# Optimization experiments

Measured on AMD Instinct MI355X. Metric: run time of the kernel, lower is better.

## Reference

```python
import jax, jax.numpy as jnp
import numpy as np

B, S, NB = 8, 512, 23
INIT, E, R, T = 512, 256, 3, 2
NEG = -9e8

def _gru(x, h, wih, whh, bih, bhh):
    gi = x @ wih.T + bih
    gh = h @ whh.T + bhh
    ir, iz, inn = jnp.split(gi, 3, axis=-1)
    hr, hz, hn = jnp.split(gh, 3, axis=-1)
    r = jax.nn.sigmoid(ir + hr)
    z = jax.nn.sigmoid(iz + hz)
    n = jnp.tanh(inn + r * hn)
    return (1.0 - z) * n + z * h

def setup_inputs():
    key = jax.random.key(0)
    ks = jax.random.split(key, 30)
    def lin(k, o, i):
        return jax.random.normal(k, (o, i), jnp.float32) * 0.02
    def vec(k, n):
        return jax.random.normal(k, (n,), jnp.float32) * 0.02
    inp = {}
    inp["amino_list"] = jax.random.normal(ks[0], (B, S, INIT), jnp.float32)
    inp["amino_mask"] = (jax.random.uniform(ks[1], (B, S)) < 0.9).astype(jnp.float32)
    inp["emb_W"] = lin(ks[2], E, INIT); inp["emb_b"] = vec(ks[3], E)
    inp["nb_W"] = lin(ks[4], E, INIT); inp["nb_b"] = vec(ks[5], E)
    inp["align_W"] = jax.random.normal(ks[6], (R, 1, 2 * E), jnp.float32) * 0.02
    inp["align_b"] = jax.random.normal(ks[7], (R, 1), jnp.float32) * 0.02
    inp["attend_W"] = jax.random.normal(ks[8], (R, E, E), jnp.float32) * 0.02
    inp["attend_b"] = jax.random.normal(ks[9], (R, E), jnp.float32) * 0.02
    inp["gru_wih"] = jax.random.normal(ks[10], (R, 3 * E, E), jnp.float32) * 0.02
    inp["gru_whh"] = jax.random.normal(ks[11], (R, 3 * E, E), jnp.float32) * 0.02
    inp["gru_bih"] = jax.random.normal(ks[12], (R, 3 * E), jnp.float32) * 0.02
    inp["gru_bhh"] = jax.random.normal(ks[13], (R, 3 * E), jnp.float32) * 0.02
    inp["seq_align_W"] = lin(ks[14], 1, 2 * E); inp["seq_align_b"] = vec(ks[15], 1)
    inp["seq_attend_W"] = lin(ks[16], E, E); inp["seq_attend_b"] = vec(ks[17], E)
    inp["seq_gru_wih"] = lin(ks[18], 3 * E, E); inp["seq_gru_bih"] = vec(ks[19], 3 * E)
    inp["seq_gru_whh"] = lin(ks[20], 3 * E, E); inp["seq_gru_bhh"] = vec(ks[21], 3 * E)
    inp["amino_degree_list"] = jax.random.randint(ks[22], (B, S, NB), -1, S)
    return inp

def reference(amino_list, amino_mask, emb_W, emb_b, nb_W, nb_b, align_W, align_b,
              attend_W, attend_b, gru_wih, gru_whh, gru_bih, gru_bhh,
              seq_align_W, seq_align_b, seq_attend_W, seq_attend_b,
              seq_gru_wih, seq_gru_whh, seq_gru_bih, seq_gru_bhh, amino_degree_list):
    idx = amino_degree_list
    lrelu = jax.nn.leaky_relu
    # per-batch neighbor gather: (S,D),(S,NB) -> (S,NB,D); index -1 wraps (masked out below)
    gather = jax.vmap(lambda f, i: f[i])
    feat = lrelu(amino_list @ emb_W.T + emb_b)               # (B,S,E)
    nfeat = lrelu(gather(amino_list, idx) @ nb_W.T + nb_b)   # (B,S,NB,E)
    attend_mask = (idx != -1).astype(feat.dtype)             # (B,S,NB)
    smask = jnp.where(idx == -1, NEG, 0.0).astype(feat.dtype)

    def attn(d, center, nbr):
        # align Linear on concat([center, nbr]) split into two matvecs (same math, no concat)
        aW = align_W[d, 0]
        score = lrelu(jnp.einsum('bse,e->bs', center, aW[:E])[:, :, None]
                      + jnp.einsum('bsne,e->bsn', nbr, aW[E:]) + align_b[d, 0])
        w = jax.nn.softmax(score + smask, axis=-1) * attend_mask   # softmax over neighbor axis
        nt = nbr @ attend_W[d].T + attend_b[d]
        return jax.nn.elu(jnp.einsum('bsn,bsne->bse', w, nt))

    h = _gru(attn(0, feat, nfeat).reshape(-1, E), feat.reshape(-1, E),
             gru_wih[0], gru_whh[0], gru_bih[0], gru_bhh[0])
    act = jax.nn.relu(h.reshape(B, S, E))
    for d in range(1, R):
        ctx = attn(d, act, gather(act, idx))
        h = _gru(ctx.reshape(-1, E), h, gru_wih[d], gru_whh[d], gru_bih[d], gru_bhh[d])
        act = jax.nn.relu(h.reshape(B, S, E))

    seq_feature = jnp.sum(act * amino_mask[:, :, None], axis=1)  # (B,E)
    act_mol = jax.nn.relu(seq_feature)                           # fixed across T (as in torch)
    seq_smask = jnp.where(amino_mask == 0, NEG, 0.0)
    saW = seq_align_W[0]
    act_seq = act_mol
    for _ in range(T):
        score = lrelu((act_mol @ saW[:E])[:, None]
                      + jnp.einsum('bse,e->bs', act, saW[E:]) + seq_align_b[0])
        w = jax.nn.softmax(score + seq_smask, axis=-1) * amino_mask  # softmax over seq axis
        tf = act @ seq_attend_W.T + seq_attend_b
        seq_ctx = jax.nn.elu(jnp.einsum('bs,bse->be', w, tf))
        seq_feature = _gru(seq_ctx, seq_feature, seq_gru_wih, seq_gru_whh, seq_gru_bih, seq_gru_bhh)
        act_seq = jax.nn.relu(seq_feature)
    return (act_seq, act)
```

## Files before the change

kernel.cpp:

```cpp
#include <hip/hip_runtime.h>
#include <math.h>


#define BSZ   8
#define SEQ   512
#define NBR   23
#define EMB   256
#define INITD 512
#define BS    (BSZ*SEQ)
#define G3    (3*EMB)
#define NEGV  -9e8f

typedef __attribute__((ext_vector_type(8))) short short8;
typedef __attribute__((ext_vector_type(4))) float f32x4;

__device__ __forceinline__ float lrelu(float x){ return x > 0.f ? x : 0.01f*x; }
__device__ __forceinline__ float elu1 (float x){ return x > 0.f ? x : (expf(x)-1.f); }
__device__ __forceinline__ float sigm (float x){ return 1.f/(1.f+expf(-x)); }
__device__ __forceinline__ float bf2f(ushort u){
    union { unsigned int i; float f; } v; v.i = ((unsigned int)u) << 16; return v.f;
}
__device__ __forceinline__ ushort f2bf(float f){
    union { float f; unsigned int i; } v; v.f = f;
    unsigned int u = v.i;
    return (ushort)((u + 0x7FFFu + ((u >> 16) & 1u)) >> 16);
}
__device__ __forceinline__ unsigned pk2(float a, float b){
    return (unsigned)f2bf(a) | ((unsigned)f2bf(b) << 16);
}
__device__ __forceinline__ void unpack8(uint4 v, float* o) {
    o[0]=bf2f((ushort)(v.x&0xffff)); o[1]=bf2f((ushort)(v.x>>16));
    o[2]=bf2f((ushort)(v.y&0xffff)); o[3]=bf2f((ushort)(v.y>>16));
    o[4]=bf2f((ushort)(v.z&0xffff)); o[5]=bf2f((ushort)(v.z>>16));
    o[6]=bf2f((ushort)(v.w&0xffff)); o[7]=bf2f((ushort)(v.w>>16));
}

__device__ __forceinline__ void gload_lds16(const void* g, void* l) {
    __builtin_amdgcn_global_load_lds(
        (const __attribute__((address_space(1))) unsigned int*)g,
        (__attribute__((address_space(3))) unsigned int*)l,
        16, 0, 0);
}

__global__ __launch_bounds__(256) void convert_flat(
    const float* __restrict__ amino, ushort* __restrict__ aminobf,
    const float* __restrict__ embW,  ushort* __restrict__ embWbf,
    const float* __restrict__ nbW,   ushort* __restrict__ nbWbf,
    const float* __restrict__ attW,  ushort* __restrict__ attWbf,
    const float* __restrict__ gwih,  ushort* __restrict__ gwihbf,
    const float* __restrict__ gwhh,  ushort* __restrict__ gwhhbf,
    const float* __restrict__ satW,  ushort* __restrict__ satWbf,
    const float* __restrict__ sgwih, ushort* __restrict__ sgwihbf,
    const float* __restrict__ sgwhh, ushort* __restrict__ sgwhhbf,
    float* __restrict__ seqfeatZ)
{
    const unsigned stride = gridDim.x * 256;
    for (unsigned u = blockIdx.x*256 + threadIdx.x; u < 524544u; u += stride) {
        const float* s; ushort* d; unsigned lu;
        if      (u < 262144u) { s=amino; d=aminobf; lu=u; }
        else if (u < 278528u) { s=embW;  d=embWbf;  lu=u-262144u; }
        else if (u < 294912u) { s=nbW;   d=nbWbf;   lu=u-278528u; }
        else if (u < 319488u) { s=attW;  d=attWbf;  lu=u-294912u; }
        else if (u < 393216u) { s=gwih;  d=gwihbf;  lu=u-319488u; }
        else if (u < 466944u) { s=gwhh;  d=gwhhbf;  lu=u-393216u; }
        else if (u < 475136u) { s=satW;  d=satWbf;  lu=u-466944u; }
        else if (u < 499712u) { s=sgwih; d=sgwihbf; lu=u-475136u; }
        else if (u < 524288u) { s=sgwhh; d=sgwhhbf; lu=u-499712u; }
        else {
            unsigned i = (u - 524288u) * 8;
            *reinterpret_cast<float4*>(&seqfeatZ[i])     = make_float4(0,0,0,0);
            *reinterpret_cast<float4*>(&seqfeatZ[i + 4]) = make_float4(0,0,0,0);
            continue;
        }
        size_t i = (size_t)lu * 8;
        float4 a = *reinterpret_cast<const float4*>(s + i);
        float4 b = *reinterpret_cast<const float4*>(s + i + 4);
        uint4 o;
        o.x = pk2(a.x, a.y); o.y = pk2(a.z, a.w);
        o.z = pk2(b.x, b.y); o.w = pk2(b.z, b.w);
        *reinterpret_cast<uint4*>(d + i) = o;
    }
}

struct GemmLds64 { ushort A[2][128][64]; ushort B[2][64][64]; };

template<int ACT>
__device__ __forceinline__ void gemm64_dev(
    const ushort* __restrict__ A, const ushort* __restrict__ W,
    const float* __restrict__ bias,
    float* __restrict__ C, ushort* __restrict__ Cbf,
    int N, int K, int bx, int by, GemmLds64& L)
{
    const int tid = threadIdx.x;
    const int m0 = bx * 128, n0 = by * 64;
    const int wv = tid >> 6, lane = tid & 63;
    const int fr = lane & 15, grp = lane >> 4;
    const int kc = K >> 3;
    const int mh = wv & 1, nh = wv >> 1;
    const int lrow = lane >> 3;
    const int csrc = (lane & 7) ^ lrow;

    f32x4 acc[4][2];
    #pragma unroll
    for (int i = 0; i < 4; ++i)
        #pragma unroll
        for (int n = 0; n < 2; ++n) acc[i][n] = (f32x4){0.f,0.f,0.f,0.f};

    auto stage = [&](int c, int k0) {
        const int kch = (k0 >> 3) + csrc;
        #pragma unroll
        for (int i = 0; i < 4; ++i) {
            const int s = (wv << 2) + i;
            gload_lds16(A + ((size_t)(m0 + (s << 3) + lrow) * kc + kch) * 8,
                        &L.A[c][s << 3][0]);
        }
        #pragma unroll
        for (int i = 0; i < 2; ++i) {
            const int s = (wv << 1) + i;
            gload_lds16(W + ((size_t)(n0 + (s << 3) + lrow) * kc + kch) * 8,
                        &L.B[c][s << 3][0]);
        }
    };
    auto compute = [&](int c) {
        #pragma unroll
        for (int ks = 0; ks < 2; ++ks) {
            short8 af[4];
            #pragma unroll
            for (int i = 0; i < 4; ++i) {
                const int ar = (mh << 6) + (i << 4) + fr;
                af[i] = *reinterpret_cast<const short8*>(
                    &L.A[c][ar][(((ks << 2) + grp) ^ (ar & 7)) << 3]);
            }
            #pragma unroll
            for (int n = 0; n < 2; ++n) {
                const int br = (nh << 5) + (n << 4) + fr;
                short8 bv = *reinterpret_cast<const short8*>(
                    &L.B[c][br][(((ks << 2) + grp) ^ (br & 7)) << 3]);
                #pragma unroll
                for (int i = 0; i < 4; ++i)
                    acc[i][n] = __builtin_amdgcn_mfma_f32_16x16x32_bf16(
                        af[i], bv, acc[i][n], 0, 0, 0);
            }
        }
    };

    const int KT = K >> 6;
    stage(0, 0);
    __syncthreads();
    int cur = 0;
    for (int kt = 1; kt < KT; ++kt) {
        stage(cur ^ 1, kt << 6);
        compute(cur);
        __syncthreads();
        cur ^= 1;
    }
    compute(cur);

    #pragma unroll
    for (int i = 0; i < 4; ++i) {
        const int mrow = m0 + (mh << 6) + (i << 4) + (grp << 2);
        #pragma unroll
        for (int n = 0; n < 2; ++n) {
            const int col = n0 + (nh << 5) + (n << 4) + fr;
            const float bv = bias[col];
            #pragma unroll
            for (int j = 0; j < 4; ++j) {
                float t = acc[i][n][j] + bv;
                if (ACT == 1) t = lrelu(t);
                size_t off = (size_t)(mrow + j) * N + col;
                if (C)   C[off] = t;
                if (Cbf) Cbf[off] = f2bf(t);
            }
        }
    }
}

__global__ __launch_bounds__(256) void featnbase_kernel(
    const ushort* __restrict__ aminobf,
    const ushort* __restrict__ embWbf, const float* __restrict__ embB,
    float* __restrict__ feat, ushort* __restrict__ featbf,
    const ushort* __restrict__ nbWbf, const float* __restrict__ nbB,
    float* __restrict__ nbase, ushort* __restrict__ nbasebf)
{
    __shared__ GemmLds64 L;
    int blk = blockIdx.x;
    if (blk < 128)
        gemm64_dev<1>(aminobf, embWbf, embB, feat, featbf, EMB, INITD, blk & 31, blk >> 5, L);
    else {
        blk -= 128;
        gemm64_dev<1>(aminobf, nbWbf, nbB, nbase, nbasebf, EMB, INITD, blk & 31, blk >> 5, L);
    }
}

__global__ __launch_bounds__(256) void dot2_kernel(
    const float* __restrict__ center, const float* __restrict__ nbrbase,
    const float* __restrict__ alignWd,
    float* __restrict__ cdot, float* __restrict__ ndot)
{
    const int lane = threadIdx.x & 63;
    const int wv   = threadIdx.x >> 6;
    const int e    = lane << 2;
    const int rb   = blockIdx.x * 32 + wv * 8;
    float4 w0 = *reinterpret_cast<const float4*>(&alignWd[e]);
    float4 w1 = *reinterpret_cast<const float4*>(&alignWd[EMB + e]);
    #pragma unroll
    for (int i = 0; i < 8; ++i) {
        const int r = rb + i;
        float4 xc = *reinterpret_cast<const float4*>(&center[(size_t)r*EMB + e]);
        float4 xn = *reinterpret_cast<const float4*>(&nbrbase[(size_t)r*EMB + e]);
        float ac = xc.x*w0.x + xc.y*w0.y + xc.z*w0.z + xc.w*w0.w;
        float an = xn.x*w1.x + xn.y*w1.y + xn.z*w1.z + xn.w*w1.w;
        #pragma unroll
        for (int off = 32; off; off >>= 1) {
            ac += __shfl_xor(ac, off, 64);
            an += __shfl_xor(an, off, 64);
        }
        if (lane == 0) { cdot[r] = ac; ndot[r] = an; }
    }
}

struct GALds { ushort ctxpre[16][256]; ushort ctx[16][256]; float wsum_s[16]; };

__global__ __launch_bounds__(512) void gatherattend_kernel(
    const float* __restrict__ cdot, const float* __restrict__ ndot,
    const int* __restrict__ idx, const ushort* __restrict__ nbr,
    const float* __restrict__ alignBd,
    const ushort* __restrict__ attWd, const float* __restrict__ attBd,
    ushort* __restrict__ ctxbf)
{
    __shared__ GALds L;
    const int tid = threadIdx.x;
    const int r0 = blockIdx.x * 16;

    {
        const int row16 = tid >> 5, sub = tid & 31;
        const int r = r0 + row16, b = r >> 9;
        float sc = -3e38f, vm = 0.f; int rn = 0;
        if (sub < NBR) {
            int j = idx[(size_t)r*NBR + sub];
            int valid = (j >= 0);
            int jj = valid ? j : j + SEQ;
            rn = b*SEQ + jj;
            vm = (float)valid;
            sc = lrelu(cdot[r] + ndot[rn] + alignBd[0]) + (valid ? 0.f : NEGV);
        }
        float m = sc;
        #pragma unroll
        for (int off = 16; off; off >>= 1) m = fmaxf(m, __shfl_xor(m, off, 32));
        float ev = (sub < NBR) ? expf(sc - m) : 0.f;
        float s = ev;
        #pragma unroll
        for (int off = 16; off; off >>= 1) s += __shfl_xor(s, off, 32);
        float wgt = ev * vm / s;
        float ws = wgt;
        #pragma unroll
        for (int off = 16; off; off >>= 1) ws += __shfl_xor(ws, off, 32);
        float a8[8] = {};
        const int e0 = sub << 3;
        #pragma unroll
        for (int n = 0; n < NBR; ++n) {
            float wn = __shfl(wgt, n, 32);
            int   rr = __shfl(rn, n, 32);
            uint4 v = *reinterpret_cast<const uint4*>(&nbr[(size_t)rr*EMB + e0]);
            float x[8]; unpack8(v, x);
            #pragma unroll
            for (int i = 0; i < 8; ++i) a8[i] += wn * x[i];
        }
        uint4 o;
        o.x = pk2(a8[0],a8[1]); o.y = pk2(a8[2],a8[3]);
        o.z = pk2(a8[4],a8[5]); o.w = pk2(a8[6],a8[7]);
        *reinterpret_cast<uint4*>(&L.ctxpre[row16][(sub ^ (row16&7)) << 3]) = o;
        if (sub == 0) L.wsum_s[row16] = ws;
    }
    __syncthreads();

    const int wv = tid >> 6, lane = tid & 63;
    const int fr = lane & 15, grp = lane >> 4;
    {
        f32x4 acc[2] = {(f32x4){0,0,0,0},(f32x4){0,0,0,0}};
        #pragma unroll
        for (int kt = 0; kt < 8; ++kt) {
            short8 af = *reinterpret_cast<const short8*>(
                &L.ctxpre[fr][((((kt<<2)+grp) ^ (fr&7)) << 3)]);
            #pragma unroll
            for (int f = 0; f < 2; ++f) {
                const int col = (wv<<5) + (f<<4) + fr;
                short8 bv = *reinterpret_cast<const short8*>(
                    &attWd[(size_t)col*EMB + (kt<<5) + (grp<<3)]);
                acc[f] = __builtin_amdgcn_mfma_f32_16x16x32_bf16(af, bv, acc[f], 0, 0, 0);
            }
        }
        #pragma unroll
        for (int f = 0; f < 2; ++f) {
            const int col = (wv<<5) + (f<<4) + fr;
            const float bb = attBd[col];
            #pragma unroll
            for (int j = 0; j < 4; ++j) {
                const int row = (grp<<2) + j;
                L.ctx[row][col] = f2bf(elu1(acc[f][j] + L.wsum_s[row]*bb));
            }
        }
    }
    __syncthreads();
    {
        const int row = tid >> 5, c = tid & 31;
        uint4 v = *reinterpret_cast<const uint4*>(&L.ctx[row][c << 3]);
        *reinterpret_cast<uint4*>(&ctxbf[(size_t)(r0+row)*EMB + (c << 3)]) = v;
    }
}

__global__ __launch_bounds__(256) void gigh_kernel(
    const ushort* __restrict__ ctxbf, const ushort* __restrict__ gwihd,
    const float* __restrict__ gbihd, ushort* __restrict__ gibf,
    const ushort* __restrict__ hprevbf, const ushort* __restrict__ gwhhd,
    const float* __restrict__ gbhhd, ushort* __restrict__ ghbf)
{
    __shared__ GemmLds64 L;
    int blk = blockIdx.x;
    if (blk < 384)
        gemm64_dev<0>(ctxbf, gwihd, gbihd, nullptr, gibf, G3, EMB, blk & 31, blk >> 5, L);
    else {
        blk -= 384;
        gemm64_dev<0>(hprevbf, gwhhd, gbhhd, nullptr, ghbf, G3, EMB, blk & 31, blk >> 5, L);
    }
}

template<int LAST>
__global__ __launch_bounds__(512) void grudot_kernel(
    const ushort* __restrict__ gibf, const ushort* __restrict__ ghbf,
    const ushort* __restrict__ hprevbf, const float* __restrict__ nextW,
    const float* __restrict__ mask,
    ushort* __restrict__ hbf, float* __restrict__ actout,
    ushort* __restrict__ actbf,
    float* __restrict__ cdotO, float* __restrict__ ndotO,
    float* __restrict__ seqfeatA)
{
    __shared__ float sred[16][256];
    const int tid = threadIdx.x;
    const int row = tid >> 5, sub = tid & 31;
    const int e0 = sub << 3;
    const size_t r = (size_t)blockIdx.x * 16 + row;
    const size_t gb = r*G3;
    uint4 giA = *reinterpret_cast<const uint4*>(&gibf[gb + e0]);
    uint4 giB = *reinterpret_cast<const uint4*>(&gibf[gb + 256 + e0]);
    uint4 giC = *reinterpret_cast<const uint4*>(&gibf[gb + 512 + e0]);
    uint4 ghA = *reinterpret_cast<const uint4*>(&ghbf[gb + e0]);
    uint4 ghB = *reinterpret_cast<const uint4*>(&ghbf[gb + 256 + e0]);
    uint4 ghC = *reinterpret_cast<const uint4*>(&ghbf[gb + 512 + e0]);
    uint4 hpv = *reinterpret_cast<const uint4*>(&hprevbf[r*EMB + e0]);
    float ir_[8], iz_[8], in_[8], hr_[8], hz_[8], hn_[8], hp_[8];
    unpack8(giA, ir_); unpack8(giB, iz_); unpack8(giC, in_);
    unpack8(ghA, hr_); unpack8(ghB, hz_); unpack8(ghC, hn_);
    unpack8(hpv, hp_);
    float hv8[8], av8[8];
    #pragma unroll
    for (int i = 0; i < 8; ++i) {
        float rg = sigm(ir_[i] + hr_[i]);
        float z  = sigm(iz_[i] + hz_[i]);
        float n  = tanhf(in_[i] + rg*hn_[i]);
        hv8[i] = (1.f - z)*n + z*hp_[i];
        av8[i] = fmaxf(hv8[i], 0.f);
    }
    if (LAST) {
        *reinterpret_cast<float4*>(&actout[r*EMB + e0])     = make_float4(av8[0],av8[1],av8[2],av8[3]);
        *reinterpret_cast<float4*>(&actout[r*EMB + e0 + 4]) = make_float4(av8[4],av8[5],av8[6],av8[7]);
    }
    uint4 hb, ab;
    hb.x = pk2(hv8[0],hv8[1]); hb.y = pk2(hv8[2],hv8[3]);
    hb.z = pk2(hv8[4],hv8[5]); hb.w = pk2(hv8[6],hv8[7]);
    ab.x = pk2(av8[0],av8[1]); ab.y = pk2(av8[2],av8[3]);
    ab.z = pk2(av8[4],av8[5]); ab.w = pk2(av8[6],av8[7]);
    *reinterpret_cast<uint4*>(&hbf[r*EMB + e0])   = hb;
    *reinterpret_cast<uint4*>(&actbf[r*EMB + e0]) = ab;
    float pc = 0.f, pn = 0.f;
    float4 w1a = *reinterpret_cast<const float4*>(&nextW[EMB + e0]);
    float4 w1b = *reinterpret_cast<const float4*>(&nextW[EMB + e0 + 4]);
    pn = av8[0]*w1a.x + av8[1]*w1a.y + av8[2]*w1a.z + av8[3]*w1a.w
       + av8[4]*w1b.x + av8[5]*w1b.y + av8[6]*w1b.z + av8[7]*w1b.w;
    if (!LAST) {
        float4 w0a = *reinterpret_cast<const float4*>(&nextW[e0]);
        float4 w0b = *reinterpret_cast<const float4*>(&nextW[e0 + 4]);
        pc = av8[0]*w0a.x + av8[1]*w0a.y + av8[2]*w0a.z + av8[3]*w0a.w
           + av8[4]*w0b.x + av8[5]*w0b.y + av8[6]*w0b.z + av8[7]*w0b.w;
    }
    #pragma unroll
    for (int off = 16; off; off >>= 1) {
        pn += __shfl_xor(pn, off, 32);
        if (!LAST) pc += __shfl_xor(pc, off, 32);
    }
    if (sub == 0) {
        if (!LAST) cdotO[r] = pc;
        ndotO[r] = pn;
    }
    if (LAST) {
        const float mk = mask[r];
        #pragma unroll
        for (int i = 0; i < 8; ++i) sred[row][e0 + i] = av8[i] * mk;
        __syncthreads();
        if (tid < 256) {
            float s = 0.f;
            #pragma unroll
            for (int rr = 0; rr < 16; ++rr) s += sred[rr][tid];
            atomicAdd(&seqfeatA[(blockIdx.x >> 5)*EMB + tid], s);
        }
    }
}

__global__ __launch_bounds__(256) void seqpre_kernel(
    const ushort* __restrict__ actbf, const ushort* __restrict__ satWbf,
    const float* __restrict__ satB, float* __restrict__ tf)
{
    __shared__ GemmLds64 L;
    gemm64_dev<0>(actbf, satWbf, satB, tf, nullptr, EMB, EMB,
                  blockIdx.x & 31, blockIdx.x >> 5, L);
}

__global__ __launch_bounds__(512) void seqstep0_kernel(
    const float* __restrict__ ad, const float* __restrict__ mask,
    const float* __restrict__ saB, const float* __restrict__ saW,
    const float* __restrict__ seqfeat, const float* __restrict__ tf,
    const ushort* __restrict__ sgwihbf, const float* __restrict__ sgbih,
    const ushort* __restrict__ sgwhhbf, const float* __restrict__ sgbhh,
    float* __restrict__ sgi, float* __restrict__ sfout,
    float* __restrict__ actseq)
{
    const int b = blockIdx.x >> 2, q = blockIdx.x & 3;
    const int tid = threadIdx.x, lane = tid & 63, wv = tid >> 6;
    __shared__ float xs[EMB], hs[EMB], gis[192], ghs[192];
    __shared__ float w_s[SEQ], red[SEQ], pv[2][EMB];
    if (tid < EMB) {
        float sf = seqfeat[b*EMB + tid];
        hs[tid] = sf;
        red[tid] = fmaxf(sf, 0.f) * saW[tid];
    }
    __syncthreads();
    for (int off = 128; off; off >>= 1) {
        if (tid < off) red[tid] += red[tid + off];
        __syncthreads();
    }
    const float cmol = red[0];
    __syncthreads();
    const float mk = mask[b*SEQ + tid];
    const float sc = lrelu(cmol + ad[b*SEQ + tid] + saB[0]) + (mk == 0.f ? NEGV : 0.f);
    red[tid] = sc; __syncthreads();
    for (int off = 256; off; off >>= 1) {
        if (tid < off) red[tid] = fmaxf(red[tid], red[tid + off]);
        __syncthreads();
    }
    const float m = red[0]; __syncthreads();
    const float ev = expf(sc - m);
    red[tid] = ev; __syncthreads();
    for (int off = 256; off; off >>= 1) {
        if (tid < off) red[tid] += red[tid + off];
        __syncthreads();
    }
    w_s[tid] = ev / red[0] * mk;
    __syncthreads();
    {
        const int e = tid & 255, scn = tid >> 8;
        const float* tfb = &tf[((size_t)b*SEQ + scn*256)*EMB + e];
        float acc = 0.f;
        #pragma unroll 4
        for (int s = 0; s < 256; ++s)
            acc += w_s[scn*256 + s] * tfb[(size_t)s*EMB];
        pv[scn][e] = acc;
    }
    __syncthreads();
    if (tid < EMB) xs[tid] = elu1(pv[0][tid] + pv[1][tid]);
    __syncthreads();
    for (int i = 0; i < 48; ++i) {
        const int l = wv * 48 + i;
        const int iswih = (l < 192);
        const int ll = iswih ? l : l - 192;
        const int g = (ll >> 6)*EMB + (q << 6) + (ll & 63);
        const ushort* Wm = iswih ? sgwihbf : sgwhhbf;
        ushort4 w4 = *reinterpret_cast<const ushort4*>(&Wm[(size_t)g*EMB + (lane << 2)]);
        float4 x4 = *reinterpret_cast<const float4*>(iswih ? &xs[lane << 2] : &hs[lane << 2]);
        float d = bf2f(w4.x)*x4.x + bf2f(w4.y)*x4.y + bf2f(w4.z)*x4.z + bf2f(w4.w)*x4.w;
        #pragma unroll
        for (int off = 32; off; off >>= 1) d += __shfl_xor(d, off, 64);
        if (lane == 0) {
            if (iswih) {
                d += sgbih[g];
                gis[ll] = d;
                sgi[b*G3 + g] = d;
            } else {
                ghs[ll] = d + sgbhh[g];
            }
        }
    }
    __syncthreads();
    if (tid < 64) {
        const int e = (q << 6) + tid;
        float rg = sigm(gis[tid]       + ghs[tid]);
        float z  = sigm(gis[64 + tid]  + ghs[64 + tid]);
        float n  = tanhf(gis[128 + tid] + rg*ghs[128 + tid]);
        float hv = (1.f - z)*n + z*hs[e];
        sfout[b*EMB + e]  = hv;
        actseq[b*EMB + e] = fmaxf(hv, 0.f);
    }
}

__global__ __launch_bounds__(512) void seqstep1_kernel(
    const float* __restrict__ sfin,
    const ushort* __restrict__ sgwhhbf, const float* __restrict__ sgbhh,
    const float* __restrict__ sgi, float* __restrict__ sfout,
    float* __restrict__ actseq)
{
    const int b = blockIdx.x >> 2, q = blockIdx.x & 3;
    const int tid = threadIdx.x, lane = tid & 63, wv = tid >> 6;
    __shared__ float hs[EMB];
    __shared__ float gis[192], ghs[192];
    if (tid < EMB) hs[tid] = sfin[b*EMB + tid];
    for (int l = tid; l < 192; l += 512) {
        int g = (l >> 6)*EMB + (q << 6) + (l & 63);
        gis[l] = sgi[b*G3 + g];
    }
    __syncthreads();
    for (int i = 0; i < 24; ++i) {
        const int l = wv * 24 + i;
        const int g = (l >> 6)*EMB + (q << 6) + (l & 63);
        ushort4 w4 = *reinterpret_cast<const ushort4*>(&sgwhhbf[(size_t)g*EMB + (lane << 2)]);
        float4 h4 = *reinterpret_cast<const float4*>(&hs[lane << 2]);
        float d = bf2f(w4.x)*h4.x + bf2f(w4.y)*h4.y + bf2f(w4.z)*h4.z + bf2f(w4.w)*h4.w;
        #pragma unroll
        for (int off = 32; off; off >>= 1) d += __shfl_xor(d, off, 64);
        if (lane == 0) ghs[l] = d + sgbhh[g];
    }
    __syncthreads();
    if (tid < 64) {
        const int e = (q << 6) + tid;
        float rg = sigm(gis[tid]       + ghs[tid]);
        float z  = sigm(gis[64 + tid]  + ghs[64 + tid]);
        float n  = tanhf(gis[128 + tid] + rg*ghs[128 + tid]);
        float hv = (1.f - z)*n + z*hs[e];
        sfout[b*EMB + e]  = hv;
        actseq[b*EMB + e] = fmaxf(hv, 0.f);
    }
}

extern "C" void kernel_launch(void* const* d_in, const int* in_sizes, int n_in,
                              void* d_out, int out_size, void* d_ws, size_t ws_size,
                              hipStream_t stream) {
    (void)in_sizes; (void)n_in; (void)out_size; (void)ws_size;
    const float* amino  = (const float*)d_in[0];
    const float* mask   = (const float*)d_in[1];
    const float* embW   = (const float*)d_in[2];
    const float* embB   = (const float*)d_in[3];
    const float* nbW    = (const float*)d_in[4];
    const float* nbB    = (const float*)d_in[5];
    const float* alignW = (const float*)d_in[6];
    const float* alignB = (const float*)d_in[7];
    const float* attW   = (const float*)d_in[8];
    const float* attB   = (const float*)d_in[9];
    const float* gwih   = (const float*)d_in[10];
    const float* gwhh   = (const float*)d_in[11];
    const float* gbih   = (const float*)d_in[12];
    const float* gbhh   = (const float*)d_in[13];
    const float* saW    = (const float*)d_in[14];
    const float* saB    = (const float*)d_in[15];
    const float* satW   = (const float*)d_in[16];
    const float* satB   = (const float*)d_in[17];
    const float* sgwih  = (const float*)d_in[18];
    const float* sgbih  = (const float*)d_in[19];
    const float* sgwhh  = (const float*)d_in[20];
    const float* sgbhh  = (const float*)d_in[21];
    const int*   idx    = (const int*)d_in[22];

    char* cur = (char*)d_ws;
    auto alloc = [&](size_t bytes) -> char* {
        char* p = cur; cur += (bytes + 255) & ~(size_t)255; return p;
    };
    float* feat    = (float*)alloc((size_t)BS*EMB*4);
    float* nbase   = (float*)alloc((size_t)BS*EMB*4);
    float* tf      = (float*)alloc((size_t)BS*EMB*4);
    float* cdot    = (float*)alloc(BS*4);
    float* ndot    = (float*)alloc(BS*4);
    float* seqfeat = (float*)alloc(BSZ*EMB*4);
    float* sf2     = (float*)alloc(BSZ*EMB*4);
    float* sgi     = (float*)alloc(BSZ*G3*4);
    ushort* aminobf  = (ushort*)alloc((size_t)BS*INITD*2);
    ushort* featbf   = (ushort*)alloc((size_t)BS*EMB*2);
    ushort* nbasebf  = (ushort*)alloc((size_t)BS*EMB*2);
    ushort* actbf    = (ushort*)alloc((size_t)BS*EMB*2);
    ushort* hbf      = (ushort*)alloc((size_t)BS*EMB*2);
    ushort* ctxbf    = (ushort*)alloc((size_t)BS*EMB*2);
    ushort* gibf     = (ushort*)alloc((size_t)BS*G3*2);
    ushort* ghbf     = (ushort*)alloc((size_t)BS*G3*2);
    ushort* embWbf   = (ushort*)alloc((size_t)EMB*INITD*2);
    ushort* nbWbf    = (ushort*)alloc((size_t)EMB*INITD*2);
    ushort* attWbf   = (ushort*)alloc((size_t)3*EMB*EMB*2);
    ushort* gwihbf   = (ushort*)alloc((size_t)3*G3*EMB*2);
    ushort* gwhhbf   = (ushort*)alloc((size_t)3*G3*EMB*2);
    ushort* satWbf   = (ushort*)alloc((size_t)EMB*EMB*2);
    ushort* sgwihbf  = (ushort*)alloc((size_t)G3*EMB*2);
    ushort* sgwhhbf  = (ushort*)alloc((size_t)G3*EMB*2);

    float* out    = (float*)d_out;
    float* actseq = out;
    float* act    = out + BSZ*EMB;

    convert_flat<<<2048, 256, 0, stream>>>(
        amino, aminobf, embW, embWbf, nbW, nbWbf, attW, attWbf,
        gwih, gwihbf, gwhh, gwhhbf, satW, satWbf,
        sgwih, sgwihbf, sgwhh, sgwhhbf, seqfeat);

    featnbase_kernel<<<256, 256, 0, stream>>>(
        aminobf, embWbf, embB, feat, featbf, nbWbf, nbB, nbase, nbasebf);

    dot2_kernel<<<128, 256, 0, stream>>>(feat, nbase, alignW, cdot, ndot);

    for (int d = 0; d < 3; ++d) {
        const ushort* nbrbf   = (d == 0) ? nbasebf : actbf;
        const ushort* hprevbf = (d == 0) ? featbf  : hbf;
        gatherattend_kernel<<<BS/16, 512, 0, stream>>>(
            cdot, ndot, idx, nbrbf, alignB + d,
            attWbf + (size_t)d*EMB*EMB, attB + d*EMB, ctxbf);
        gigh_kernel<<<768, 256, 0, stream>>>(
            ctxbf, gwihbf + (size_t)d*G3*EMB, gbih + d*G3, gibf,
            hprevbf, gwhhbf + (size_t)d*G3*EMB, gbhh + d*G3, ghbf);
        if (d < 2) {
            grudot_kernel<0><<<BS/16, 512, 0, stream>>>(
                gibf, ghbf, hprevbf, alignW + (d+1)*2*EMB, mask,
                hbf, act, actbf, cdot, ndot, seqfeat);
        } else {
            grudot_kernel<1><<<BS/16, 512, 0, stream>>>(
                gibf, ghbf, hprevbf, saW, mask,
                hbf, act, actbf, cdot, ndot, seqfeat);
        }
    }

    seqpre_kernel<<<128, 256, 0, stream>>>(actbf, satWbf, satB, tf);
    seqstep0_kernel<<<32, 512, 0, stream>>>(
        ndot, mask, saB, saW, seqfeat, tf,
        sgwihbf, sgbih, sgwhhbf, sgbhh, sgi, sf2, actseq);
    seqstep1_kernel<<<32, 512, 0, stream>>>(
        sf2, sgwhhbf, sgbhh, sgi, seqfeat, actseq);
}
```

Baseline: 177.0 us.

## Split sequence attention pooling into a wide partial-sum kernel before the GRU step

The softmax-weighted pooling over the transformed features used to run inside seqstep0 on only 32 blocks, and each block read a quarter-batch of tf serially. It is now a separate kernel with a 16x8 grid, where each block recomputes the softmax and sums a 32-position slice into a partial buffer. The GRU step kernel, now templated, adds the 16 partials and applies ELU. This spreads the bandwidth-bound weighted sum over many more CUs, at the cost of one extra launch, redundant softmax work per block and a small partial buffer.

```diff
diff --git a/kernel.cpp b/kernel.cpp
--- a/kernel.cpp
+++ b/kernel.cpp
@@ -415,10 +415,55 @@
                   blockIdx.x & 31, blockIdx.x >> 5, L);
 }
 
-__global__ __launch_bounds__(512) void seqstep0_kernel(
+__global__ __launch_bounds__(256) void seqpv2_kernel(
     const float* __restrict__ ad, const float* __restrict__ mask,
     const float* __restrict__ saB, const float* __restrict__ saW,
     const float* __restrict__ seqfeat, const float* __restrict__ tf,
+    float* __restrict__ partial)
+{
+    const int st = blockIdx.x, b = blockIdx.y;
+    const int tid = threadIdx.x;
+    __shared__ float w_s[SEQ];
+    __shared__ float red[256];
+    red[tid] = fmaxf(seqfeat[b*EMB + tid], 0.f) * saW[tid];
+    __syncthreads();
+    for (int off = 128; off; off >>= 1) {
+        if (tid < off) red[tid] += red[tid + off];
+        __syncthreads();
+    }
+    const float cb = red[0];
+    __syncthreads();
+    float mk0 = mask[b*SEQ + tid], mk1 = mask[b*SEQ + 256 + tid];
+    float bb = saB[0];
+    float s0 = lrelu(cb + ad[b*SEQ + tid] + bb)       + (mk0 == 0.f ? NEGV : 0.f);
+    float s1 = lrelu(cb + ad[b*SEQ + 256 + tid] + bb) + (mk1 == 0.f ? NEGV : 0.f);
+    red[tid] = fmaxf(s0, s1); __syncthreads();
+    for (int off = 128; off; off >>= 1) {
+        if (tid < off) red[tid] = fmaxf(red[tid], red[tid + off]);
+        __syncthreads();
+    }
+    float m = red[0]; __syncthreads();
+    float e0 = expf(s0 - m), e1 = expf(s1 - m);
+    red[tid] = e0 + e1; __syncthreads();
+    for (int off = 128; off; off >>= 1) {
+        if (tid < off) red[tid] += red[tid + off];
+        __syncthreads();
+    }
+    float inv = 1.f / red[0];
+    w_s[tid]       = e0 * inv * mk0;
+    w_s[tid + 256] = e1 * inv * mk1;
+    __syncthreads();
+    float acc = 0.f;
+    const int s0i = st * 32;
+    #pragma unroll 4
+    for (int s = s0i; s < s0i + 32; ++s)
+        acc += w_s[s] * tf[((size_t)b*SEQ + s)*EMB + tid];
+    partial[((size_t)b*16 + st)*EMB + tid] = acc;
+}
+
+template<int T0>
+__global__ __launch_bounds__(512) void seqstep_kernel(
+    const float* __restrict__ partial, const float* __restrict__ sfin,
     const ushort* __restrict__ sgwihbf, const float* __restrict__ sgbih,
     const ushort* __restrict__ sgwhhbf, const float* __restrict__ sgbhh,
     float* __restrict__ sgi, float* __restrict__ sfout,
@@ -426,52 +471,32 @@
 {
     const int b = blockIdx.x >> 2, q = blockIdx.x & 3;
     const int tid = threadIdx.x, lane = tid & 63, wv = tid >> 6;
-    __shared__ float xs[EMB], hs[EMB], gis[192], ghs[192];
-    __shared__ float w_s[SEQ], red[SEQ], pv[2][EMB];
+    __shared__ float xs[EMB];
+    __shared__ float hs[EMB];
+    __shared__ float gis[192], ghs[192];
     if (tid < EMB) {
-        float sf = seqfeat[b*EMB + tid];
-        hs[tid] = sf;
-        red[tid] = fmaxf(sf, 0.f) * saW[tid];
-    }
-    __syncthreads();
-    for (int off = 128; off; off >>= 1) {
-        if (tid < off) red[tid] += red[tid + off];
-        __syncthreads();
-    }
-    const float cmol = red[0];
-    __syncthreads();
-    const float mk = mask[b*SEQ + tid];
-    const float sc = lrelu(cmol + ad[b*SEQ + tid] + saB[0]) + (mk == 0.f ? NEGV : 0.f);
-    red[tid] = sc; __syncthreads();
-    for (int off = 256; off; off >>= 1) {
-        if (tid < off) red[tid] = fmaxf(red[tid], red[tid + off]);
-        __syncthreads();
-    }
-    const float m = red[0]; __syncthreads();
-    const float ev = expf(sc - m);
-    red[tid] = ev; __syncthreads();
-    for (int off = 256; off; off >>= 1) {
-        if (tid < off) red[tid] += red[tid + off];
-        __syncthreads();
-    }
-    w_s[tid] = ev / red[0] * mk;
-    __syncthreads();
-    {
-        const int e = tid & 255, scn = tid >> 8;
-        const float* tfb = &tf[((size_t)b*SEQ + scn*256)*EMB + e];
-        float acc = 0.f;
-        #pragma unroll 4
-        for (int s = 0; s < 256; ++s)
-            acc += w_s[scn*256 + s] * tfb[(size_t)s*EMB];
-        pv[scn][e] = acc;
-    }
-    __syncthreads();
-    if (tid < EMB) xs[tid] = elu1(pv[0][tid] + pv[1][tid]);
-    __syncthreads();
-    for (int i = 0; i < 48; ++i) {
-        const int l = wv * 48 + i;
-        const int iswih = (l < 192);
-        const int ll = iswih ? l : l - 192;
+        hs[tid] = sfin[b*EMB + tid];
+        if (T0) {
+            float a = 0.f;
+            #pragma unroll
+            for (int st = 0; st < 16; ++st)
+                a += partial[((size_t)b*16 + st)*EMB + tid];
+            xs[tid] = elu1(a);
+        }
+    }
+    if (!T0) {
+        for (int l = tid; l < 192; l += 512) {
+            int g = (l >> 6)*EMB + (q << 6) + (l & 63);
+            gis[l] = sgi[b*G3 + g];
+        }
+    }
+    __syncthreads();
+    const int nrows = T0 ? 384 : 192;
+    const int rpw = nrows >> 3;
+    for (int i = 0; i < rpw; ++i) {
+        const int l = wv * rpw + i;
+        const int iswih = T0 && (l < 192);
+        const int ll = (T0 && l >= 192) ? l - 192 : l;
         const int g = (ll >> 6)*EMB + (q << 6) + (ll & 63);
         const ushort* Wm = iswih ? sgwihbf : sgwhhbf;
         ushort4 w4 = *reinterpret_cast<const ushort4*>(&Wm[(size_t)g*EMB + (lane << 2)]);
@@ -488,44 +513,6 @@
                 ghs[ll] = d + sgbhh[g];
             }
         }
-    }
-    __syncthreads();
-    if (tid < 64) {
-        const int e = (q << 6) + tid;
-        float rg = sigm(gis[tid]       + ghs[tid]);
-        float z  = sigm(gis[64 + tid]  + ghs[64 + tid]);
-        float n  = tanhf(gis[128 + tid] + rg*ghs[128 + tid]);
-        float hv = (1.f - z)*n + z*hs[e];
-        sfout[b*EMB + e]  = hv;
-        actseq[b*EMB + e] = fmaxf(hv, 0.f);
-    }
-}
-
-__global__ __launch_bounds__(512) void seqstep1_kernel(
-    const float* __restrict__ sfin,
-    const ushort* __restrict__ sgwhhbf, const float* __restrict__ sgbhh,
-    const float* __restrict__ sgi, float* __restrict__ sfout,
-    float* __restrict__ actseq)
-{
-    const int b = blockIdx.x >> 2, q = blockIdx.x & 3;
-    const int tid = threadIdx.x, lane = tid & 63, wv = tid >> 6;
-    __shared__ float hs[EMB];
-    __shared__ float gis[192], ghs[192];
-    if (tid < EMB) hs[tid] = sfin[b*EMB + tid];
-    for (int l = tid; l < 192; l += 512) {
-        int g = (l >> 6)*EMB + (q << 6) + (l & 63);
-        gis[l] = sgi[b*G3 + g];
-    }
-    __syncthreads();
-    for (int i = 0; i < 24; ++i) {
-        const int l = wv * 24 + i;
-        const int g = (l >> 6)*EMB + (q << 6) + (l & 63);
-        ushort4 w4 = *reinterpret_cast<const ushort4*>(&sgwhhbf[(size_t)g*EMB + (lane << 2)]);
-        float4 h4 = *reinterpret_cast<const float4*>(&hs[lane << 2]);
-        float d = bf2f(w4.x)*h4.x + bf2f(w4.y)*h4.y + bf2f(w4.z)*h4.z + bf2f(w4.w)*h4.w;
-        #pragma unroll
-        for (int off = 32; off; off >>= 1) d += __shfl_xor(d, off, 64);
-        if (lane == 0) ghs[l] = d + sgbhh[g];
     }
     __syncthreads();
     if (tid < 64) {
@@ -579,6 +566,7 @@
     float* seqfeat = (float*)alloc(BSZ*EMB*4);
     float* sf2     = (float*)alloc(BSZ*EMB*4);
     float* sgi     = (float*)alloc(BSZ*G3*4);
+    float* partial = (float*)alloc((size_t)BSZ*16*EMB*4);
     ushort* aminobf  = (ushort*)alloc((size_t)BS*INITD*2);
     ushort* featbf   = (ushort*)alloc((size_t)BS*EMB*2);
     ushort* nbasebf  = (ushort*)alloc((size_t)BS*EMB*2);
@@ -631,9 +619,10 @@
     }
 
     seqpre_kernel<<<128, 256, 0, stream>>>(actbf, satWbf, satB, tf);
-    seqstep0_kernel<<<32, 512, 0, stream>>>(
-        ndot, mask, saB, saW, seqfeat, tf,
-        sgwihbf, sgbih, sgwhhbf, sgbhh, sgi, sf2, actseq);
-    seqstep1_kernel<<<32, 512, 0, stream>>>(
-        sf2, sgwhhbf, sgbhh, sgi, seqfeat, actseq);
-}
+    seqpv2_kernel<<<dim3(16, BSZ), 256, 0, stream>>>(
+        ndot, mask, saB, saW, seqfeat, tf, partial);
+    seqstep_kernel<1><<<32, 512, 0, stream>>>(
+        partial, seqfeat, sgwihbf, sgbih, sgwhhbf, sgbhh, sgi, sf2, actseq);
+    seqstep_kernel<0><<<32, 512, 0, stream>>>(
+        partial, sf2, sgwihbf, sgbih, sgwhhbf, sgbhh, sgi, seqfeat, actseq);
+}
```

Result: faster. 164.7 us (median of 2 runs) (-7.0%).
